# Optimization experiments

Measured on AMD Instinct MI355X. Metric: run time of the kernel, lower is better.

The kernel has to match this reference:

```python
import jax, jax.numpy as jnp
import numpy as np

N_RAYS, N_SAMPLES, HIDDEN, N_VOXELS = 8192, 256, 64, 1000


def setup_inputs() -> dict:
    key = jax.random.key(0)
    ks = jax.random.split(key, 10)
    ray_start = jax.random.normal(ks[0], (N_RAYS, 3), jnp.float32)
    ray_dir = jax.random.normal(ks[1], (N_RAYS, 3), jnp.float32)
    ray_dir = ray_dir / jnp.linalg.norm(ray_dir, axis=-1, keepdims=True)
    # monotonically increasing depths along each ray
    sampled_depth = jnp.sort(jax.random.uniform(ks[2], (N_RAYS, N_SAMPLES), jnp.float32) * 4.0 + 0.5, axis=-1)
    sampled_dists = jax.random.uniform(ks[3], (N_RAYS, N_SAMPLES), jnp.float32) * 0.02 + 1e-3
    sampled_idx = jax.random.randint(ks[4], (N_RAYS, N_SAMPLES), -333, N_VOXELS).astype(jnp.int64)
    W1 = jax.random.normal(ks[5], (3, HIDDEN), jnp.float32) * 0.5
    b1 = jnp.zeros((HIDDEN,), jnp.float32)
    w_sigma = jax.random.normal(ks[6], (HIDDEN,), jnp.float32) * 0.5
    W_rgb = jax.random.normal(ks[7], (HIDDEN, 3), jnp.float32) * 0.5
    W_dir = jax.random.normal(ks[8], (3, 3), jnp.float32) * 0.5
    b_rgb = jnp.zeros((3,), jnp.float32)
    return {"ray_start": ray_start, "ray_dir": ray_dir, "sampled_depth": sampled_depth,
            "sampled_dists": sampled_dists, "sampled_idx": sampled_idx,
            "W1": W1, "b1": b1, "w_sigma": w_sigma, "W_rgb": W_rgb, "W_dir": W_dir, "b_rgb": b_rgb}


def _volume_render(ray_start, ray_dir, sampled_depth, sampled_dists, sampled_idx,
                   W1, b1, w_sigma, W_rgb, W_dir, b_rgb):
    # sampled_xyz = ray(ray_start, ray_dir, depth)
    xyz = ray_start[:, None, :] + ray_dir[:, None, :] * sampled_depth[..., None]  # [N,P,3]
    h = jax.nn.relu(jnp.einsum('npi,ih->nph', xyz, W1) + b1)                      # [N,P,H]
    sigma = jnp.einsum('nph,h->np', h, w_sigma)                                   # [N,P]
    rgb = jax.nn.sigmoid(jnp.einsum('nph,hc->npc', h, W_rgb)
                         + jnp.einsum('ni,ic->nc', ray_dir, W_dir)[:, None, :] + b_rgb)  # [N,P,3]
    mask = (sampled_idx != -1).astype(sigma.dtype)                                # [N,P]
    # free_energy = relu(sigma) * dists * 7.0, scattered back with zeros at misses
    free_energy = jax.nn.relu(sigma) * sampled_dists * 7.0 * mask
    shifted = jnp.concatenate([jnp.zeros_like(free_energy[:, :1]), free_energy[:, :-1]], axis=-1)
    a = 1.0 - jnp.exp(-free_energy)
    b = jnp.exp(-jnp.cumsum(shifted, axis=-1))
    probs = a * b                                                                 # [N,P]
    depths = jnp.sum(sampled_depth * probs, axis=-1)                              # [N]
    missed = 1.0 - jnp.sum(probs, axis=-1)                                        # [N]
    colors = jnp.sum(rgb * probs[..., None], axis=-2)                             # [N,3]
    return jnp.concatenate([colors, depths[:, None], missed[:, None], probs], axis=-1)  # [N, 3+1+1+P]


def reference(ray_start, ray_dir, sampled_depth, sampled_dists, sampled_idx,
              W1, b1, w_sigma, W_rgb, W_dir, b_rgb):
    return _volume_render(ray_start, ray_dir, sampled_depth, sampled_dists, sampled_idx,
                          W1, b1, w_sigma, W_rgb, W_dir, b_rgb)
```

## Files before the change

### kernel.cpp

```cpp
#include <hip/hip_runtime.h>

#define NRAYS 8192
#define NS    256
#define HID   64
#define RPB   4
#define EP    260

typedef _Float16 f16x2 __attribute__((ext_vector_type(2)));
typedef _Float16 f16x8 __attribute__((ext_vector_type(8)));
typedef float    f32x4 __attribute__((ext_vector_type(4)));

#define WAVE_LDS_FENCE() asm volatile("s_waitcnt lgkmcnt(0)" ::: "memory")

__global__ __launch_bounds__(256) void vr_kernel(
    const float* __restrict__ ray_start,
    const float* __restrict__ ray_dir,
    const float* __restrict__ sampled_depth,
    const float* __restrict__ sampled_dists,
    const int*   __restrict__ sampled_idx,
    const float* __restrict__ W1,
    const float* __restrict__ b1,
    const float* __restrict__ w_sigma,
    const float* __restrict__ W_rgb,
    const float* __restrict__ W_dir,
    const float* __restrict__ b_rgb,
    float* __restrict__ out)
{
    __shared__ _Float16 sA[RPB][HID];
    __shared__ _Float16 sB[RPB][HID];
    __shared__ _Float16 sDep[RPB][NS];
    __shared__ float    sE[RPB][4][EP];

    const int t    = threadIdx.x;
    const int lane = t & 63;
    const int wv   = t >> 6;
    const int ray  = blockIdx.x * RPB + wv;

    const float ox = ray_start[ray*3+0], oy = ray_start[ray*3+1], oz = ray_start[ray*3+2];
    const float dx = ray_dir[ray*3+0],  dy = ray_dir[ray*3+1],  dz = ray_dir[ray*3+2];
    {
        const int h = lane;
        const float w0 = W1[h], w1 = W1[HID + h], w2 = W1[2*HID + h];
        const float A = fmaf(w0, ox, fmaf(w1, oy, fmaf(w2, oz, b1[h])));
        const float B = fmaf(w0, dx, fmaf(w1, dy, w2 * dz));
        sA[wv][h] = (_Float16)A;
        sB[wv][h] = (_Float16)B;
    }

    const float dwr = fmaf(dx, W_dir[0], fmaf(dy, W_dir[3], fmaf(dz, W_dir[6], b_rgb[0])));
    const float dwg = fmaf(dx, W_dir[1], fmaf(dy, W_dir[4], fmaf(dz, W_dir[7], b_rgb[1])));
    const float dwb = fmaf(dx, W_dir[2], fmaf(dy, W_dir[5], fmaf(dz, W_dir[8], b_rgb[2])));

    const size_t rbase = (size_t)ray * NS + (size_t)lane * 4;
    const float4 dep = *(const float4*)(sampled_depth + rbase);
    const float4 dst = *(const float4*)(sampled_dists + rbase);
    const int4  vidx = *(const int4*)(sampled_idx + rbase);

    {
        f16x2 dl; dl.x = (_Float16)dep.x; dl.y = (_Float16)dep.y;
        f16x2 dh; dh.x = (_Float16)dep.z; dh.y = (_Float16)dep.w;
        f16x2* dp = (f16x2*)&sDep[wv][4*lane];
        dp[0] = dl; dp[1] = dh;
    }

    const int n = lane & 15;
    const int q = lane >> 4;
    f16x8 bflo = (f16x8)(_Float16)0.f;
    f16x8 bfhi = (f16x8)(_Float16)0.f;
    if (n < 4) {
#pragma unroll
        for (int j = 0; j < 8; ++j) {
            const int klo = q*8 + j, khi = 32 + q*8 + j;
            const float vlo = (n == 0) ? w_sigma[klo] : W_rgb[klo*3 + (n-1)];
            const float vhi = (n == 0) ? w_sigma[khi] : W_rgb[khi*3 + (n-1)];
            bflo[j] = (_Float16)vlo;
            bfhi[j] = (_Float16)vhi;
        }
    }

    WAVE_LDS_FENCE();

    const f16x8 Alo = *(const f16x8*)&sA[wv][q*8];
    const f16x8 Ahi = *(const f16x8*)&sA[wv][32 + q*8];
    const f16x8 Blo = *(const f16x8*)&sB[wv][q*8];
    const f16x8 Bhi = *(const f16x8*)&sB[wv][32 + q*8];
    const f16x8 z8  = (f16x8)(_Float16)0.f;

#pragma unroll
    for (int tt = 0; tt < 16; ++tt) {
        const _Float16 dv = sDep[wv][16*tt + n];
        f16x8 d8;
#pragma unroll
        for (int j = 0; j < 8; ++j) d8[j] = dv;
        f16x8 hlo = __builtin_elementwise_fma(Blo, d8, Alo);
        f16x8 hhi = __builtin_elementwise_fma(Bhi, d8, Ahi);
        hlo = __builtin_elementwise_max(hlo, z8);
        hhi = __builtin_elementwise_max(hhi, z8);
        f32x4 acc = {0.f, 0.f, 0.f, 0.f};
        acc = __builtin_amdgcn_mfma_f32_16x16x32_f16(hlo, bflo, acc, 0, 0, 0);
        acc = __builtin_amdgcn_mfma_f32_16x16x32_f16(hhi, bfhi, acc, 0, 0, 0);
        if (n < 4)
            *(f32x4*)&sE[wv][n][16*tt + 4*q] = acc;
    }

    WAVE_LDS_FENCE();

    const f32x4 sg4 = *(const f32x4*)&sE[wv][0][4*lane];
    const f32x4 cr4 = *(const f32x4*)&sE[wv][1][4*lane];
    const f32x4 cg4 = *(const f32x4*)&sE[wv][2][4*lane];
    const f32x4 cb4 = *(const f32x4*)&sE[wv][3][4*lane];

    const float dpt[4] = {dep.x, dep.y, dep.z, dep.w};
    const float dsv[4] = {dst.x, dst.y, dst.z, dst.w};
    const int   vid[4] = {vidx.x, vidx.y, vidx.z, vidx.w};

    float c[4];
    float run = 0.f;
#pragma unroll
    for (int j = 0; j < 4; ++j) {
        float f = fmaxf(sg4[j], 0.f) * dsv[j] * 7.0f;
        if (vid[j] == -1) f = 0.f;
        run += f;
        c[j] = run;
    }

    float tot = run;
#pragma unroll
    for (int off = 1; off < 64; off <<= 1) {
        const float v = __shfl_up(tot, off, 64);
        if (lane >= off) tot += v;
    }
    const float base = tot - run;

    float Eprev = __expf(-base);
    float prob[4];
    float s0 = 0.f, s1 = 0.f, s2 = 0.f, s3 = 0.f, s4 = 0.f;
#pragma unroll
    for (int j = 0; j < 4; ++j) {
        const float Ej = __expf(-(base + c[j]));
        const float p  = Eprev - Ej;
        Eprev = Ej;
        prob[j] = p;
        const float rr = __builtin_amdgcn_rcpf(1.f + __expf(-(cr4[j] + dwr)));
        const float gg = __builtin_amdgcn_rcpf(1.f + __expf(-(cg4[j] + dwg)));
        const float bb = __builtin_amdgcn_rcpf(1.f + __expf(-(cb4[j] + dwb)));
        s0 += p;
        s1 = fmaf(dpt[j], p, s1);
        s2 = fmaf(rr, p, s2);
        s3 = fmaf(gg, p, s3);
        s4 = fmaf(bb, p, s4);
    }

    float* orow = out + (size_t)ray * (NS + 5);
#pragma unroll
    for (int j = 0; j < 4; ++j)
        orow[5 + 4*lane + j] = prob[j];

#pragma unroll
    for (int off = 32; off >= 1; off >>= 1) {
        s0 += __shfl_xor(s0, off, 64);
        s1 += __shfl_xor(s1, off, 64);
        s2 += __shfl_xor(s2, off, 64);
        s3 += __shfl_xor(s3, off, 64);
        s4 += __shfl_xor(s4, off, 64);
    }

    if (lane == 0) {
        orow[0] = s2;
        orow[1] = s3;
        orow[2] = s4;
        orow[3] = s1;
        orow[4] = 1.f - s0;
    }
}

extern "C" void kernel_launch(void* const* d_in, const int* in_sizes, int n_in,
                              void* d_out, int out_size, void* d_ws, size_t ws_size,
                              hipStream_t stream)
{
    vr_kernel<<<NRAYS / RPB, 256, 0, stream>>>(
        (const float*)d_in[0],
        (const float*)d_in[1],
        (const float*)d_in[2],
        (const float*)d_in[3],
        (const int*)  d_in[4],
        (const float*)d_in[5],
        (const float*)d_in[6],
        (const float*)d_in[7],
        (const float*)d_in[8],
        (const float*)d_in[9],
        (const float*)d_in[10],
        (float*)d_out);
}
```

Measured before the change: 104.8 us.

## Split per-ray projection and weight packing into a separate prep kernel

Moves the per-ray A/B hidden-layer projection, the direction colour term and the fp16 MFMA weight fragments into a prep kernel that writes them to workspace. The main kernel then loads these as vectors instead of computing them and doing scattered weight loads in every wave. This removes redundant per-block weight gathers, but adds a second kernel launch and a workspace round trip. The fused kernel is kept as a fallback when the workspace is too small.

After: 106.6 us. Within noise of the previous version (+1.7%).

```diff
diff --git a/kernel.cpp b/kernel.cpp
--- a/kernel.cpp
+++ b/kernel.cpp
@@ -12,7 +12,184 @@
 
 #define WAVE_LDS_FENCE() asm volatile("s_waitcnt lgkmcnt(0)" ::: "memory")
 
-__global__ __launch_bounds__(256) void vr_kernel(
+__global__ __launch_bounds__(256) void prep_kernel(
+    const float* __restrict__ ray_start,
+    const float* __restrict__ ray_dir,
+    const float* __restrict__ W1,
+    const float* __restrict__ b1,
+    const float* __restrict__ w_sigma,
+    const float* __restrict__ W_rgb,
+    const float* __restrict__ W_dir,
+    const float* __restrict__ b_rgb,
+    _Float16* __restrict__ AB,
+    float* __restrict__ dw,
+    _Float16* __restrict__ WB)
+{
+    const int t   = threadIdx.x;
+    const int ray = blockIdx.x * 4 + (t >> 6);
+    const int h   = t & 63;
+
+    const float ox = ray_start[ray*3+0], oy = ray_start[ray*3+1], oz = ray_start[ray*3+2];
+    const float dx = ray_dir[ray*3+0],  dy = ray_dir[ray*3+1],  dz = ray_dir[ray*3+2];
+    const float w0 = W1[h], w1 = W1[HID + h], w2 = W1[2*HID + h];
+    const float A = fmaf(w0, ox, fmaf(w1, oy, fmaf(w2, oz, b1[h])));
+    const float B = fmaf(w0, dx, fmaf(w1, dy, w2 * dz));
+    AB[ray*128 + h]      = (_Float16)A;
+    AB[ray*128 + 64 + h] = (_Float16)B;
+
+    if (h < 3)
+        dw[ray*4 + h] = fmaf(dx, W_dir[0*3+h], fmaf(dy, W_dir[1*3+h],
+                         fmaf(dz, W_dir[2*3+h], b_rgb[h])));
+
+    if (blockIdx.x == 0 && t < 128) {
+        const int j = t & 7, n = (t >> 3) & 3, q = t >> 5;
+        const int klo = q*8 + j, khi = 32 + q*8 + j;
+        const float vlo = (n == 0) ? w_sigma[klo] : W_rgb[klo*3 + (n-1)];
+        const float vhi = (n == 0) ? w_sigma[khi] : W_rgb[khi*3 + (n-1)];
+        WB[(q*4 + n)*8 + j]       = (_Float16)vlo;
+        WB[128 + (q*4 + n)*8 + j] = (_Float16)vhi;
+    }
+}
+
+__global__ __launch_bounds__(256) void vr_split(
+    const float* __restrict__ sampled_depth,
+    const float* __restrict__ sampled_dists,
+    const int*   __restrict__ sampled_idx,
+    const _Float16* __restrict__ AB,
+    const float* __restrict__ dw,
+    const _Float16* __restrict__ WB,
+    float* __restrict__ out)
+{
+    __shared__ _Float16 sDep[RPB][NS];
+    __shared__ float    sE[RPB][4][EP];
+
+    const int t    = threadIdx.x;
+    const int lane = t & 63;
+    const int wv   = t >> 6;
+    const int ray  = blockIdx.x * RPB + wv;
+    const int n    = lane & 15;
+    const int q    = lane >> 4;
+
+    const _Float16* abr = AB + (size_t)ray * 128;
+    const f16x8 Alo = *(const f16x8*)(abr + q*8);
+    const f16x8 Ahi = *(const f16x8*)(abr + 32 + q*8);
+    const f16x8 Blo = *(const f16x8*)(abr + 64 + q*8);
+    const f16x8 Bhi = *(const f16x8*)(abr + 96 + q*8);
+
+    f16x8 bflo = (f16x8)(_Float16)0.f;
+    f16x8 bfhi = (f16x8)(_Float16)0.f;
+    if (n < 4) {
+        bflo = *(const f16x8*)(WB + (q*4 + n)*8);
+        bfhi = *(const f16x8*)(WB + 128 + (q*4 + n)*8);
+    }
+
+    const float dwr = dw[ray*4 + 0];
+    const float dwg = dw[ray*4 + 1];
+    const float dwb = dw[ray*4 + 2];
+
+    const size_t rbase = (size_t)ray * NS + (size_t)lane * 4;
+    const float4 dep = *(const float4*)(sampled_depth + rbase);
+    const float4 dst = *(const float4*)(sampled_dists + rbase);
+    const int4  vidx = *(const int4*)(sampled_idx + rbase);
+
+    {
+        f16x2 dl; dl.x = (_Float16)dep.x; dl.y = (_Float16)dep.y;
+        f16x2 dh; dh.x = (_Float16)dep.z; dh.y = (_Float16)dep.w;
+        f16x2* dp = (f16x2*)&sDep[wv][4*lane];
+        dp[0] = dl; dp[1] = dh;
+    }
+    WAVE_LDS_FENCE();
+
+    const f16x8 z8 = (f16x8)(_Float16)0.f;
+
+#pragma unroll
+    for (int tt = 0; tt < 16; ++tt) {
+        const _Float16 dv = sDep[wv][16*tt + n];
+        f16x8 d8;
+#pragma unroll
+        for (int j = 0; j < 8; ++j) d8[j] = dv;
+        f16x8 hlo = __builtin_elementwise_fma(Blo, d8, Alo);
+        f16x8 hhi = __builtin_elementwise_fma(Bhi, d8, Ahi);
+        hlo = __builtin_elementwise_max(hlo, z8);
+        hhi = __builtin_elementwise_max(hhi, z8);
+        f32x4 acc = {0.f, 0.f, 0.f, 0.f};
+        acc = __builtin_amdgcn_mfma_f32_16x16x32_f16(hlo, bflo, acc, 0, 0, 0);
+        acc = __builtin_amdgcn_mfma_f32_16x16x32_f16(hhi, bfhi, acc, 0, 0, 0);
+        if (n < 4)
+            *(f32x4*)&sE[wv][n][16*tt + 4*q] = acc;
+    }
+    WAVE_LDS_FENCE();
+
+    const f32x4 sg4 = *(const f32x4*)&sE[wv][0][4*lane];
+    const f32x4 cr4 = *(const f32x4*)&sE[wv][1][4*lane];
+    const f32x4 cg4 = *(const f32x4*)&sE[wv][2][4*lane];
+    const f32x4 cb4 = *(const f32x4*)&sE[wv][3][4*lane];
+
+    const float dpt[4] = {dep.x, dep.y, dep.z, dep.w};
+    const float dsv[4] = {dst.x, dst.y, dst.z, dst.w};
+    const int   vid[4] = {vidx.x, vidx.y, vidx.z, vidx.w};
+
+    float c[4];
+    float run = 0.f;
+#pragma unroll
+    for (int j = 0; j < 4; ++j) {
+        float f = fmaxf(sg4[j], 0.f) * dsv[j] * 7.0f;
+        if (vid[j] == -1) f = 0.f;
+        run += f;
+        c[j] = run;
+    }
+
+    float tot = run;
+#pragma unroll
+    for (int off = 1; off < 64; off <<= 1) {
+        const float v = __shfl_up(tot, off, 64);
+        if (lane >= off) tot += v;
+    }
+    const float base = tot - run;
+
+    float Eprev = __expf(-base);
+    float prob[4];
+    float s0 = 0.f, s1 = 0.f, s2 = 0.f, s3 = 0.f, s4 = 0.f;
+#pragma unroll
+    for (int j = 0; j < 4; ++j) {
+        const float Ej = __expf(-(base + c[j]));
+        const float p  = Eprev - Ej;
+        Eprev = Ej;
+        prob[j] = p;
+        const float rr = __builtin_amdgcn_rcpf(1.f + __expf(-(cr4[j] + dwr)));
+        const float gg = __builtin_amdgcn_rcpf(1.f + __expf(-(cg4[j] + dwg)));
+        const float bb = __builtin_amdgcn_rcpf(1.f + __expf(-(cb4[j] + dwb)));
+        s0 += p;
+        s1 = fmaf(dpt[j], p, s1);
+        s2 = fmaf(rr, p, s2);
+        s3 = fmaf(gg, p, s3);
+        s4 = fmaf(bb, p, s4);
+    }
+
+    float* orow = out + (size_t)ray * (NS + 5);
+#pragma unroll
+    for (int j = 0; j < 4; ++j)
+        orow[5 + 4*lane + j] = prob[j];
+
+#pragma unroll
+    for (int off = 32; off >= 1; off >>= 1) {
+        s0 += __shfl_xor(s0, off, 64);
+        s1 += __shfl_xor(s1, off, 64);
+        s2 += __shfl_xor(s2, off, 64);
+        s3 += __shfl_xor(s3, off, 64);
+        s4 += __shfl_xor(s4, off, 64);
+    }
+
+    if (lane == 0) {
+        orow[0] = s2;
+        orow[1] = s3;
+        orow[2] = s4;
+        orow[3] = s1;
+        orow[4] = 1.f - s0;
+    }
+}
+
+__global__ __launch_bounds__(256) void vr_fused(
     const float* __restrict__ ray_start,
     const float* __restrict__ ray_dir,
     const float* __restrict__ sampled_depth,
@@ -178,17 +355,31 @@
                               void* d_out, int out_size, void* d_ws, size_t ws_size,
                               hipStream_t stream)
 {
-    vr_kernel<<<NRAYS / RPB, 256, 0, stream>>>(
-        (const float*)d_in[0],
-        (const float*)d_in[1],
-        (const float*)d_in[2],
-        (const float*)d_in[3],
-        (const int*)  d_in[4],
-        (const float*)d_in[5],
-        (const float*)d_in[6],
-        (const float*)d_in[7],
-        (const float*)d_in[8],
-        (const float*)d_in[9],
-        (const float*)d_in[10],
-        (float*)d_out);
+    const size_t NEED = 2u*1024u*1024u + 128u*1024u + 512u;
+
+    if (d_ws != nullptr && ws_size >= NEED) {
+        char* ws = (char*)d_ws;
+        _Float16* AB  = (_Float16*)ws;
+        float*    dwv = (float*)(ws + 2u*1024u*1024u);
+        _Float16* WB  = (_Float16*)(ws + 2u*1024u*1024u + 128u*1024u);
+
+        prep_kernel<<<NRAYS / 4, 256, 0, stream>>>(
+            (const float*)d_in[0], (const float*)d_in[1],
+            (const float*)d_in[5], (const float*)d_in[6],
+            (const float*)d_in[7], (const float*)d_in[8],
+            (const float*)d_in[9], (const float*)d_in[10],
+            AB, dwv, WB);
+
+        vr_split<<<NRAYS / RPB, 256, 0, stream>>>(
+            (const float*)d_in[2], (const float*)d_in[3], (const int*)d_in[4],
+            AB, dwv, WB, (float*)d_out);
+    } else {
+        vr_fused<<<NRAYS / RPB, 256, 0, stream>>>(
+            (const float*)d_in[0], (const float*)d_in[1],
+            (const float*)d_in[2], (const float*)d_in[3], (const int*)d_in[4],
+            (const float*)d_in[5], (const float*)d_in[6],
+            (const float*)d_in[7], (const float*)d_in[8],
+            (const float*)d_in[9], (const float*)d_in[10],
+            (float*)d_out);
+    }
 }
```
